# Performance work log

Measured on AMD Instinct MI355X. Metric: run time of the kernel, lower is better.

## Reference

```python
import jax, jax.numpy as jnp
import numpy as np

N = 16000        # nodes
E = 256000       # edges
D_IN = 1280      # input node features
HID = 256        # hidden dim (all hidden_dims equal; required by res_linear shapes)
HEADS = 8
C = HID // HEADS # 32 channels per head
G = 32           # graphs in the batch
O = 64           # output labels (GO terms)
NB = 2           # conv blocks = len(hidden_dims) - 1
EPS = 1e-5


def _bn(h, g, b):
    # eval-mode BatchNorm1d with running_mean=0, running_var=1 (init state)
    return h * (g / jnp.sqrt(1.0 + EPS)) + b


def _seg_softmax(logits, seg, num):
    # numerically-stable segment softmax (PyG softmax semantics)
    m = jax.ops.segment_max(logits, seg, num_segments=num)
    e = jnp.exp(logits - m[seg])
    s = jax.ops.segment_sum(e, seg, num_segments=num)
    return e / (s[seg] + 1e-16)


def setup_inputs() -> dict:
    key = jax.random.key(0)
    ks = jax.random.split(key, 16)
    w = lambda i, sh: jax.random.normal(ks[i], sh, jnp.float32) * 0.05
    return {
        "x": jax.random.normal(ks[0], (N, D_IN), jnp.float32),
        "edge_index": jax.random.randint(ks[1], (2, E), 0, N),
        "batch": jnp.sort(jax.random.randint(ks[2], (N,), 0, G)),
        # feature_proj: Linear -> ReLU -> BN
        "fp_W": w(3, (D_IN, HID)), "fp_b": jnp.zeros(HID),
        "fp_g": jnp.ones(HID), "fp_be": jnp.zeros(HID),
        # GATv2Conv per block: lin_l, lin_r, att, out-bias
        "gat_Wl": w(4, (NB, HID, HID)), "gat_bl": jnp.zeros((NB, HID)),
        "gat_Wr": w(5, (NB, HID, HID)), "gat_br": jnp.zeros((NB, HID)),
        "gat_att": w(6, (NB, HEADS, C)), "gat_bias": jnp.zeros((NB, HID)),
        # GINConv MLP: Linear -> ReLU -> BN
        "gin_W": w(7, (NB, HID, HID)), "gin_b": jnp.zeros((NB, HID)),
        "gin_g": jnp.ones((NB, HID)), "gin_be": jnp.zeros((NB, HID)),
        # PyG LayerNorm (graph mode) affine
        "ln_g": jnp.ones((NB, HID)), "ln_b": jnp.zeros((NB, HID)),
        # residual linears
        "res_W": w(8, (NB, HID, HID)), "res_b": jnp.zeros((NB, HID)),
        # GlobalAttention gate MLP
        "pool_W1": w(9, (HID, HID)), "pool_b1": jnp.zeros(HID),
        "pool_W2": w(10, (HID, 1)), "pool_b2": jnp.zeros(1),
        # O label heads (hierarchy=None -> just the MLP), stacked
        "head_W1": w(11, (O, HID, 256)), "head_b1": jnp.zeros((O, 256)),
        "head_g": jnp.ones((O, 256)), "head_be": jnp.zeros((O, 256)),
        "head_W2": w(12, (O, 256)), "head_b2": jnp.zeros(O),
    }


def reference(x, edge_index, batch, fp_W, fp_b, fp_g, fp_be,
              gat_Wl, gat_bl, gat_Wr, gat_br, gat_att, gat_bias,
              gin_W, gin_b, gin_g, gin_be, ln_g, ln_b, res_W, res_b,
              pool_W1, pool_b1, pool_W2, pool_b2,
              head_W1, head_b1, head_g, head_be, head_W2, head_b2):
    n = x.shape[0]
    # feature_proj (eval: dropout = identity)
    h = _bn(jax.nn.relu(x @ fp_W + fp_b), fp_g, fp_be)

    src0, dst0 = edge_index[0], edge_index[1]
    loop = jnp.arange(n)
    src = jnp.concatenate([src0, loop])  # GATv2 adds self-loops by default
    dst = jnp.concatenate([dst0, loop])

    for i in range(NB):
        # ---- GATv2Conv (no activation after, per original control flow) ----
        xl = (h @ gat_Wl[i] + gat_bl[i]).reshape(n, HEADS, C)
        xr = (h @ gat_Wr[i] + gat_br[i]).reshape(n, HEADS, C)
        msg = xl[src]                                   # [E', H, C]
        eact = jax.nn.leaky_relu(msg + xr[dst], 0.2)
        logit = jnp.einsum('ehc,hc->eh', eact, gat_att[i])
        alpha = _seg_softmax(logit, dst, n)             # [E', H]
        h = jax.ops.segment_sum(alpha[:, :, None] * msg, dst,
                                num_segments=n).reshape(n, HID) + gat_bias[i]
        # ---- GINConv: nn((1+0)*x + sum_neighbors), then leaky_relu ----
        agg = jax.ops.segment_sum(h[src0], dst0, num_segments=n)
        gin = _bn(jax.nn.relu((h + agg) @ gin_W[i] + gin_b[i]), gin_g[i], gin_be[i])
        h = jax.nn.leaky_relu(gin, 0.2)
        # ---- PyG LayerNorm (graph mode, batch=None: global mean/std) + residual ----
        mu = h.mean()
        sd = jnp.std(h)
        ln = (h - mu) / (sd + EPS) * ln_g[i] + ln_b[i]
        h = jax.nn.leaky_relu(ln + (h @ res_W[i] + res_b[i]), 0.2)

    # ---- GlobalAttention pooling ----
    gate = jnp.tanh(h @ pool_W1 + pool_b1) @ pool_W2 + pool_b2   # [N, 1]
    a = _seg_softmax(gate[:, 0], batch, G)
    emb = jax.ops.segment_sum(a[:, None] * h, batch, num_segments=G)  # [G, HID]

    # ---- O label heads (hierarchy None -> MLP only), vectorized ----
    z = jnp.einsum('bd,odh->boh', emb, head_W1) + head_b1[None]
    z = _bn(jax.nn.silu(z), head_g[None], head_be[None])
    out = jnp.einsum('boh,oh->bo', z, head_W2) + head_b2[None]
    return out[:, :, None]  # torch.stack(outputs, dim=1) -> [G, O, 1]
```

## Files before the change

kernel.cpp:

```cpp
#include <hip/hip_runtime.h>
#include <math.h>

#define N_NODES 16000
#define N_EDGES 256000
#define EPE (N_EDGES + N_NODES)
#define DIN 1280
#define HID 256
#define HEADS 8
#define CPH 32
#define NG 32
#define NO 64
#define EPSC 1e-5f
#define SPAD 40

typedef __bf16 bf16;
typedef __attribute__((ext_vector_type(8))) __bf16 bf16x8;
typedef __attribute__((ext_vector_type(4))) float floatx4;

__device__ __forceinline__ float lrelu(float v) { return v > 0.f ? v : 0.2f * v; }
__device__ __forceinline__ float bflo(unsigned int u) { return __uint_as_float(u << 16); }
__device__ __forceinline__ float bfhi(unsigned int u) { return __uint_as_float(u & 0xffff0000u); }
__device__ __forceinline__ unsigned int bfpack(float x, float y) {
    bf16 b0 = (bf16)x, b1 = (bf16)y;
    return ((unsigned int)*(unsigned short*)&b0) | (((unsigned int)*(unsigned short*)&b1) << 16);
}

__device__ __forceinline__ void barrier_lds() {
    asm volatile("s_waitcnt lgkmcnt(0)" ::: "memory");
    __builtin_amdgcn_s_barrier();
}

__global__ void wconv_gen(const float* __restrict__ W, bf16* __restrict__ Wt, int K, int total) {
    int idx = blockIdx.x * 256 + threadIdx.x;
    if (idx >= total) return;
    int per = K * HID;
    int l = idx / per, rem = idx - l * per;
    int n = rem / K, k = rem - n * K;
    Wt[idx] = (bf16)W[(size_t)l * per + (size_t)k * HID + n];
}

__global__ void wconv_pair(const float* __restrict__ Wl, const float* __restrict__ Wr,
                           bf16* __restrict__ Wt) {
    int idx = blockIdx.x * 256 + threadIdx.x;
    int n = idx >> 8, k = idx & 255;
    float v = (n < 256) ? Wl[(size_t)k * HID + n] : Wr[(size_t)k * HID + (n - 256)];
    Wt[idx] = (bf16)v;
}

__global__ __launch_bounds__(256) void gemm128(
    const bf16* __restrict__ A, const bf16* __restrict__ Bt,
    const float* __restrict__ bias, const float* __restrict__ bias2,
    bf16* __restrict__ C, int K, int ldc, int mode,
    const float* __restrict__ g, const float* __restrict__ be,
    float2* __restrict__ statp, const float* __restrict__ stat)
{
    __shared__ __align__(16) bf16 As[2][128 * SPAD];
    __shared__ __align__(16) bf16 Bs[2][128 * SPAD];
    const int tid = threadIdx.x;
    const int bm = blockIdx.y * 128, bn = blockIdx.x * 128;
    const int w = tid >> 6, lane = tid & 63;
    const int wm = (w & 1) * 64, wn = (w >> 1) * 64;
    const int lrow = lane & 15, lk8 = (lane >> 4) * 8;

    floatx4 acc[4][4];
#pragma unroll
    for (int i = 0; i < 4; i++)
#pragma unroll
        for (int j = 0; j < 4; j++) acc[i][j] = (floatx4){0.f, 0.f, 0.f, 0.f};

    const int r2 = tid >> 1, c2 = tid & 1;
    const bf16* gA = A + (size_t)(bm + r2) * K + c2 * 16;
    const bf16* gB = Bt + (size_t)(bn + r2) * K + c2 * 16;
    bf16* sA = &As[0][r2 * SPAD + c2 * 16];
    bf16* sB = &Bs[0][r2 * SPAD + c2 * 16];

    const int nk = K >> 5;
    bf16x8 a[4][2], b[4][2];
#pragma unroll
    for (int u = 0; u < 4; u++) {
        const bf16* pa = gA + u * 32;
        a[u][0] = *(const bf16x8*)(pa + 0);
        a[u][1] = *(const bf16x8*)(pa + 8);
        const bf16* pb = gB + u * 32;
        b[u][0] = *(const bf16x8*)(pb + 0);
        b[u][1] = *(const bf16x8*)(pb + 8);
    }

    for (int it0 = 0; it0 < nk; it0 += 4) {
#pragma unroll
        for (int u = 0; u < 4; u++) {
            const int it = it0 + u;
            const int p = u & 1;
            const int po = p * 128 * SPAD;
            *(bf16x8*)(sA + po + 0) = a[u][0];
            *(bf16x8*)(sA + po + 8) = a[u][1];
            *(bf16x8*)(sB + po + 0) = b[u][0];
            *(bf16x8*)(sB + po + 8) = b[u][1];
            barrier_lds();
            if (it + 4 < nk) {
                const bf16* pa = gA + (it + 4) * 32;
                a[u][0] = *(const bf16x8*)(pa + 0);
                a[u][1] = *(const bf16x8*)(pa + 8);
                const bf16* pb = gB + (it + 4) * 32;
                b[u][0] = *(const bf16x8*)(pb + 0);
                b[u][1] = *(const bf16x8*)(pb + 8);
            }
            bf16x8 af[4], bfr[4];
#pragma unroll
            for (int i = 0; i < 4; i++) af[i] = *(const bf16x8*)&As[p][(wm + 16 * i + lrow) * SPAD + lk8];
#pragma unroll
            for (int j = 0; j < 4; j++) bfr[j] = *(const bf16x8*)&Bs[p][(wn + 16 * j + lrow) * SPAD + lk8];
#pragma unroll
            for (int i = 0; i < 4; i++)
#pragma unroll
                for (int j = 0; j < 4; j++)
                    acc[i][j] = __builtin_amdgcn_mfma_f32_16x16x32_bf16(af[i], bfr[j], acc[i][j], 0, 0, 0);
            barrier_lds();
        }
    }

    const float inv = rsqrtf(1.f + EPSC);
    float mu = 0.f, rs = 0.f;
    if (mode == 3) {
        const float inv_n = 1.f / (float)((size_t)N_NODES * HID);
        mu = stat[0] * inv_n;
        float var = stat[1] * inv_n - mu * mu;
        rs = 1.f / (sqrtf(fmaxf(var, 0.f)) + EPSC);
    }
    float sz = 0.f, sq = 0.f;
#pragma unroll
    for (int j = 0; j < 4; j++) {
        int col = bn + wn + 16 * j + lrow;
        float bcol = (col < HID) ? bias[col] : bias2[col - HID];
        float gc = (mode >= 2) ? g[col] : 0.f;
        float bec = (mode >= 2) ? be[col] : 0.f;
#pragma unroll
        for (int i = 0; i < 4; i++) {
            int row0 = bm + wm + 16 * i + (lane >> 4) * 4;
#pragma unroll
            for (int r = 0; r < 4; r++) {
                float z = acc[i][j][r] + bcol;
                if (mode == 2) {
                    z = fmaxf(z, 0.f) * (gc * inv) + bec;
                    z = lrelu(z);
                    sz += z; sq += z * z;
                } else if (mode == 3) {
                    float h = (float)A[(size_t)(row0 + r) * K + col];
                    z = (h - mu) * rs * gc + bec + z;
                    z = lrelu(z);
                }
                C[(size_t)(row0 + r) * ldc + col] = (bf16)z;
            }
        }
    }
    if (mode == 2) {
        for (int o = 32; o > 0; o >>= 1) { sz += __shfl_down(sz, o); sq += __shfl_down(sq, o); }
        __syncthreads();
        float* rs_ = (float*)&As[0][0];
        float* rq_ = (float*)&Bs[0][0];
        if (lane == 0) { rs_[w] = sz; rq_[w] = sq; }
        __syncthreads();
        if (tid == 0)
            statp[blockIdx.y * gridDim.x + blockIdx.x] =
                make_float2(rs_[0] + rs_[1] + rs_[2] + rs_[3],
                            rq_[0] + rq_[1] + rq_[2] + rq_[3]);
    }
}

__global__ __launch_bounds__(256, 1) void gemm_f32A(
    const float* __restrict__ A, const bf16* __restrict__ Bt,
    const float* __restrict__ bias, bf16* __restrict__ C, int K,
    const float* __restrict__ g, const float* __restrict__ be)
{
    __shared__ __align__(16) bf16 As[2][128 * SPAD];
    __shared__ __align__(16) bf16 Bs[2][128 * SPAD];
    const int tid = threadIdx.x;
    const int bm = blockIdx.y * 128, bn = blockIdx.x * 128;
    const int w = tid >> 6, lane = tid & 63;
    const int wm = (w & 1) * 64, wn = (w >> 1) * 64;
    const int lrow = lane & 15, lk8 = (lane >> 4) * 8;

    floatx4 acc[4][4];
#pragma unroll
    for (int i = 0; i < 4; i++)
#pragma unroll
        for (int j = 0; j < 4; j++) acc[i][j] = (floatx4){0.f, 0.f, 0.f, 0.f};

    const int r2 = tid >> 1, c2 = tid & 1;
    const float* gA = A + (size_t)(bm + r2) * K + c2 * 16;
    const bf16* gB = Bt + (size_t)(bn + r2) * K + c2 * 16;
    bf16* sA = &As[0][r2 * SPAD + c2 * 16];
    bf16* sB = &Bs[0][r2 * SPAD + c2 * 16];

    const int nk = K >> 5;
    float4 a[4][4];
    bf16x8 b[4][2];
#pragma unroll
    for (int u = 0; u < 4; u++) {
        const float* pa = gA + u * 32;
        a[u][0] = *(const float4*)(pa + 0);
        a[u][1] = *(const float4*)(pa + 4);
        a[u][2] = *(const float4*)(pa + 8);
        a[u][3] = *(const float4*)(pa + 12);
        const bf16* pb = gB + u * 32;
        b[u][0] = *(const bf16x8*)(pb + 0);
        b[u][1] = *(const bf16x8*)(pb + 8);
    }

    for (int it0 = 0; it0 < nk; it0 += 4) {
#pragma unroll
        for (int u = 0; u < 4; u++) {
            const int it = it0 + u;
            const int p = u & 1;
            const int po = p * 128 * SPAD;
            bf16x8 h0, h1;
            h0[0] = (bf16)a[u][0].x; h0[1] = (bf16)a[u][0].y; h0[2] = (bf16)a[u][0].z; h0[3] = (bf16)a[u][0].w;
            h0[4] = (bf16)a[u][1].x; h0[5] = (bf16)a[u][1].y; h0[6] = (bf16)a[u][1].z; h0[7] = (bf16)a[u][1].w;
            h1[0] = (bf16)a[u][2].x; h1[1] = (bf16)a[u][2].y; h1[2] = (bf16)a[u][2].z; h1[3] = (bf16)a[u][2].w;
            h1[4] = (bf16)a[u][3].x; h1[5] = (bf16)a[u][3].y; h1[6] = (bf16)a[u][3].z; h1[7] = (bf16)a[u][3].w;
            *(bf16x8*)(sA + po + 0) = h0;
            *(bf16x8*)(sA + po + 8) = h1;
            *(bf16x8*)(sB + po + 0) = b[u][0];
            *(bf16x8*)(sB + po + 8) = b[u][1];
            barrier_lds();
            if (it + 4 < nk) {
                const float* pa = gA + (it + 4) * 32;
                a[u][0] = *(const float4*)(pa + 0);
                a[u][1] = *(const float4*)(pa + 4);
                a[u][2] = *(const float4*)(pa + 8);
                a[u][3] = *(const float4*)(pa + 12);
                const bf16* pb = gB + (it + 4) * 32;
                b[u][0] = *(const bf16x8*)(pb + 0);
                b[u][1] = *(const bf16x8*)(pb + 8);
            }
            bf16x8 af[4], bfr[4];
#pragma unroll
            for (int i = 0; i < 4; i++) af[i] = *(const bf16x8*)&As[p][(wm + 16 * i + lrow) * SPAD + lk8];
#pragma unroll
            for (int j = 0; j < 4; j++) bfr[j] = *(const bf16x8*)&Bs[p][(wn + 16 * j + lrow) * SPAD + lk8];
#pragma unroll
            for (int i = 0; i < 4; i++)
#pragma unroll
                for (int j = 0; j < 4; j++)
                    acc[i][j] = __builtin_amdgcn_mfma_f32_16x16x32_bf16(af[i], bfr[j], acc[i][j], 0, 0, 0);
            barrier_lds();
        }
    }

    const float inv = rsqrtf(1.f + EPSC);
#pragma unroll
    for (int j = 0; j < 4; j++) {
        int col = bn + wn + 16 * j + lrow;
        float bcol = bias[col];
        float gc = g[col] * inv;
        float bec = be[col];
#pragma unroll
        for (int i = 0; i < 4; i++) {
            int row0 = bm + wm + 16 * i + (lane >> 4) * 4;
#pragma unroll
            for (int r = 0; r < 4; r++) {
                float z = fmaxf(acc[i][j][r] + bcol, 0.f) * gc + bec;
                C[(size_t)(row0 + r) * HID + col] = (bf16)z;
            }
        }
    }
}

__global__ void hist_kernel(const int* __restrict__ ei, int* __restrict__ cnt) {
    int e = blockIdx.x * 256 + threadIdx.x;
    if (e >= EPE) return;
    int d = (e < N_EDGES) ? ei[N_EDGES + e] : (e - N_EDGES);
    atomicAdd(&cnt[d], 1);
}

__global__ __launch_bounds__(1024) void scan_kernel(const int* __restrict__ cnt,
                                                    int* __restrict__ roff, int* __restrict__ cursor,
                                                    const int* __restrict__ batch,
                                                    int* __restrict__ gstart) {
    __shared__ int wsum[16];
    int t = threadIdx.x;
    int base = t * 16;
    int local[16]; int s = 0;
#pragma unroll
    for (int i = 0; i < 16; i++) {
        int idx = base + i;
        int v = (idx < N_NODES) ? cnt[idx] : 0;
        local[i] = s; s += v;
    }
    int lane = t & 63, wid = t >> 6;
    int incl = s;
    for (int o = 1; o < 64; o <<= 1) { int v = __shfl_up(incl, o); if (lane >= o) incl += v; }
    if (lane == 63) wsum[wid] = incl;
    __syncthreads();
    if (t == 0) { int a = 0; for (int k = 0; k < 16; k++) { int v = wsum[k]; wsum[k] = a; a += v; } }
    __syncthreads();
    int texcl = incl - s + wsum[wid];
#pragma unroll
    for (int i = 0; i < 16; i++) {
        int idx = base + i;
        if (idx < N_NODES) { int o = texcl + local[i]; roff[idx] = o; cursor[idx] = o; }
    }
    if (t == 1023) roff[N_NODES] = texcl + s;
    if (t <= NG) {
        int lo = 0, hi = N_NODES;
        while (lo < hi) { int mid = (lo + hi) >> 1; if (batch[mid] < t) lo = mid + 1; else hi = mid; }
        gstart[t] = lo;
    }
}

__global__ void scatter_kernel(const int* __restrict__ ei, int* __restrict__ cursor,
                               int* __restrict__ esrc) {
    int e = blockIdx.x * 256 + threadIdx.x;
    if (e >= EPE) return;
    int s, d;
    if (e < N_EDGES) { s = ei[e]; d = ei[N_EDGES + e]; }
    else { s = d = e - N_EDGES; }
    int pos = atomicAdd(&cursor[d], 1);
    esrc[pos] = s;
}

__global__ __launch_bounds__(256) void gat_wave(
    const bf16* __restrict__ XLR, const int* __restrict__ roff, const int* __restrict__ esrc,
    const float* __restrict__ att, const float* __restrict__ gbias, bf16* __restrict__ out)
{
    const int wid = threadIdx.x >> 6;
    const int lane = threadIdx.x & 63;
    const int d = blockIdx.x * 4 + wid;
    const int beg = roff[d], end = roff[d + 1];
    const int c0 = lane * 4;

    const unsigned int* xru = (const unsigned int*)(XLR + (size_t)d * 512 + 256 + c0);
    const unsigned int xr01 = xru[0], xr23 = xru[1];
    const float xr0 = bflo(xr01), xr1 = bfhi(xr01), xr2 = bflo(xr23), xr3 = bfhi(xr23);
    const float at0 = att[c0], at1 = att[c0 + 1], at2 = att[c0 + 2], at3 = att[c0 + 3];

    float m = -INFINITY, s = 0.f;
    float a0 = 0.f, a1 = 0.f, a2 = 0.f, a3 = 0.f;

    int e = beg;
    for (; e + 3 < end; e += 4) {
        int s0 = esrc[e], s1 = esrc[e + 1], s2 = esrc[e + 2], s3 = esrc[e + 3];
        const unsigned int* q0 = (const unsigned int*)(XLR + (size_t)s0 * 512 + c0);
        const unsigned int* q1 = (const unsigned int*)(XLR + (size_t)s1 * 512 + c0);
        const unsigned int* q2 = (const unsigned int*)(XLR + (size_t)s2 * 512 + c0);
        const unsigned int* q3 = (const unsigned int*)(XLR + (size_t)s3 * 512 + c0);
        unsigned int u01 = q0[0], u23 = q0[1];
        unsigned int v01 = q1[0], v23 = q1[1];
        unsigned int w01 = q2[0], w23 = q2[1];
        unsigned int x01 = q3[0], x23 = q3[1];
        float x0 = bflo(u01), x1 = bfhi(u01), x2 = bflo(u23), x3 = bfhi(u23);
        float y0 = bflo(v01), y1 = bfhi(v01), y2 = bflo(v23), y3 = bfhi(v23);
        float z0 = bflo(w01), z1 = bfhi(w01), z2 = bflo(w23), z3 = bfhi(w23);
        float t0 = bflo(x01), t1 = bfhi(x01), t2 = bflo(x23), t3 = bfhi(x23);
        float p0 = lrelu(x0 + xr0) * at0 + lrelu(x1 + xr1) * at1
                 + lrelu(x2 + xr2) * at2 + lrelu(x3 + xr3) * at3;
        float p1 = lrelu(y0 + xr0) * at0 + lrelu(y1 + xr1) * at1
                 + lrelu(y2 + xr2) * at2 + lrelu(y3 + xr3) * at3;
        float p2 = lrelu(z0 + xr0) * at0 + lrelu(z1 + xr1) * at1
                 + lrelu(z2 + xr2) * at2 + lrelu(z3 + xr3) * at3;
        float p3 = lrelu(t0 + xr0) * at0 + lrelu(t1 + xr1) * at1
                 + lrelu(t2 + xr2) * at2 + lrelu(t3 + xr3) * at3;
        p0 += __shfl_xor(p0, 1);  p1 += __shfl_xor(p1, 1);
        p2 += __shfl_xor(p2, 1);  p3 += __shfl_xor(p3, 1);
        p0 += __shfl_xor(p0, 2);  p1 += __shfl_xor(p1, 2);
        p2 += __shfl_xor(p2, 2);  p3 += __shfl_xor(p3, 2);
        p0 += __shfl_xor(p0, 4);  p1 += __shfl_xor(p1, 4);
        p2 += __shfl_xor(p2, 4);  p3 += __shfl_xor(p3, 4);
        float mn = fmaxf(fmaxf(m, fmaxf(p0, p1)), fmaxf(p2, p3));
        float rsc = __expf(m - mn);
        float w0 = __expf(p0 - mn);
        float w1 = __expf(p1 - mn);
        float w2 = __expf(p2 - mn);
        float w3 = __expf(p3 - mn);
        s = s * rsc + (w0 + w1) + (w2 + w3);
        a0 = a0 * rsc + (w0 * x0 + w1 * y0) + (w2 * z0 + w3 * t0);
        a1 = a1 * rsc + (w0 * x1 + w1 * y1) + (w2 * z1 + w3 * t1);
        a2 = a2 * rsc + (w0 * x2 + w1 * y2) + (w2 * z2 + w3 * t2);
        a3 = a3 * rsc + (w0 * x3 + w1 * y3) + (w2 * z3 + w3 * t3);
        m = mn;
    }
    for (; e < end; ++e) {
        int s0 = esrc[e];
        const unsigned int* q0 = (const unsigned int*)(XLR + (size_t)s0 * 512 + c0);
        unsigned int u01 = q0[0], u23 = q0[1];
        float x0 = bflo(u01), x1 = bfhi(u01), x2 = bflo(u23), x3 = bfhi(u23);
        float p = lrelu(x0 + xr0) * at0 + lrelu(x1 + xr1) * at1
                + lrelu(x2 + xr2) * at2 + lrelu(x3 + xr3) * at3;
        p += __shfl_xor(p, 1);
        p += __shfl_xor(p, 2);
        p += __shfl_xor(p, 4);
        float mn = fmaxf(m, p);
        float rsc = __expf(m - mn);
        float wgt = __expf(p - mn);
        s = s * rsc + wgt;
        a0 = a0 * rsc + wgt * x0;
        a1 = a1 * rsc + wgt * x1;
        a2 = a2 * rsc + wgt * x2;
        a3 = a3 * rsc + wgt * x3;
        m = mn;
    }

    const float rinv = 1.f / (s + 1e-16f);
    float v0 = gbias[c0]     + a0 * rinv;
    float v1 = gbias[c0 + 1] + a1 * rinv;
    float v2 = gbias[c0 + 2] + a2 * rinv;
    float v3 = gbias[c0 + 3] + a3 * rinv;
    unsigned int* op = (unsigned int*)(out + (size_t)d * HID + c0);
    op[0] = bfpack(v0, v1);
    op[1] = bfpack(v2, v3);
}

__global__ __launch_bounds__(256) void gin_wave(
    const bf16* __restrict__ H, const int* __restrict__ roff,
    const int* __restrict__ esrc, bf16* __restrict__ U)
{
    const int wid = threadIdx.x >> 6;
    const int lane = threadIdx.x & 63;
    const int d = blockIdx.x * 4 + wid;
    const int beg = roff[d], end = roff[d + 1];
    const int c0 = lane * 4;

    float a0 = 0.f, a1 = 0.f, a2 = 0.f, a3 = 0.f;
    int e = beg;
    for (; e + 3 < end; e += 4) {
        int s0 = esrc[e], s1 = esrc[e + 1], s2 = esrc[e + 2], s3 = esrc[e + 3];
        const unsigned int* p0 = (const unsigned int*)(H + (size_t)s0 * HID + c0);
        const unsigned int* p1 = (const unsigned int*)(H + (size_t)s1 * HID + c0);
        const unsigned int* p2 = (const unsigned int*)(H + (size_t)s2 * HID + c0);
        const unsigned int* p3 = (const unsigned int*)(H + (size_t)s3 * HID + c0);
        unsigned int u01 = p0[0], u23 = p0[1];
        unsigned int v01 = p1[0], v23 = p1[1];
        unsigned int w01 = p2[0], w23 = p2[1];
        unsigned int x01 = p3[0], x23 = p3[1];
        a0 += (bflo(u01) + bflo(v01)) + (bflo(w01) + bflo(x01));
        a1 += (bfhi(u01) + bfhi(v01)) + (bfhi(w01) + bfhi(x01));
        a2 += (bflo(u23) + bflo(v23)) + (bflo(w23) + bflo(x23));
        a3 += (bfhi(u23) + bfhi(v23)) + (bfhi(w23) + bfhi(x23));
    }
    for (; e < end; ++e) {
        const unsigned int* p0 = (const unsigned int*)(H + (size_t)esrc[e] * HID + c0);
        unsigned int u01 = p0[0], u23 = p0[1];
        a0 += bflo(u01); a1 += bfhi(u01); a2 += bflo(u23); a3 += bfhi(u23);
    }
    unsigned int* up = (unsigned int*)(U + (size_t)d * HID + c0);
    up[0] = bfpack(a0, a1);
    up[1] = bfpack(a2, a3);
}

__global__ void stats_reduce(const float2* __restrict__ part, float* __restrict__ stat, int n) {
    int t = threadIdx.x;
    float s = 0.f, q = 0.f;
    for (int i = t; i < n; i += 256) { float2 v = part[i]; s += v.x; q += v.y; }
    for (int o = 32; o > 0; o >>= 1) { s += __shfl_down(s, o); q += __shfl_down(q, o); }
    __shared__ float ls[4], lq[4];
    int wid = t >> 6, lane = t & 63;
    if (lane == 0) { ls[wid] = s; lq[wid] = q; }
    __syncthreads();
    if (t == 0) { stat[0] = ls[0] + ls[1] + ls[2] + ls[3]; stat[1] = lq[0] + lq[1] + lq[2] + lq[3]; }
}

__global__ __launch_bounds__(256) void pool_gate_kernel(const bf16* __restrict__ t,
    const float* __restrict__ W2, const float* __restrict__ b2, float* __restrict__ gate)
{
    int n = blockIdx.x * 4 + (threadIdx.x >> 6);
    int lane = threadIdx.x & 63;
    const bf16* p = t + (size_t)n * HID + lane * 4;
    float4 w = *(const float4*)(W2 + lane * 4);
    float s = tanhf((float)p[0]) * w.x + tanhf((float)p[1]) * w.y
            + tanhf((float)p[2]) * w.z + tanhf((float)p[3]) * w.w;
    for (int o = 32; o > 0; o >>= 1) s += __shfl_down(s, o);
    if (lane == 0) gate[n] = s + b2[0];
}

__global__ __launch_bounds__(256) void pool_stats_kernel(
    float* __restrict__ gate, const int* __restrict__ gstart)
{
    int g = blockIdx.x, t = threadIdx.x;
    int lo = gstart[g], hi = gstart[g + 1];
    __shared__ float red[256];
    float m = -INFINITY;
    for (int n = lo + t; n < hi; n += 256) m = fmaxf(m, gate[n]);
    red[t] = m; __syncthreads();
    for (int st = 128; st > 0; st >>= 1) { if (t < st) red[t] = fmaxf(red[t], red[t + st]); __syncthreads(); }
    m = red[0]; __syncthreads();
    float s = 0.f;
    for (int n = lo + t; n < hi; n += 256) s += __expf(gate[n] - m);
    red[t] = s; __syncthreads();
    for (int st = 128; st > 0; st >>= 1) { if (t < st) red[t] += red[t + st]; __syncthreads(); }
    float sinv = 1.f / (red[0] + 1e-16f);
    for (int n = lo + t; n < hi; n += 256) gate[n] = __expf(gate[n] - m) * sinv;
}

__global__ __launch_bounds__(256) void emb_accum_kernel(
    const float* __restrict__ a, const int* __restrict__ batch,
    const bf16* __restrict__ h, float* __restrict__ emb)
{
    int n0 = blockIdx.x * 32, t = threadIdx.x;
    int cur = batch[n0]; float acc = 0.f;
    for (int j = 0; j < 32; j++) {
        int n = n0 + j;
        int b = batch[n];
        if (b != cur) { atomicAdd(&emb[cur * HID + t], acc); cur = b; acc = 0.f; }
        acc += a[n] * (float)h[(size_t)n * HID + t];
    }
    atomicAdd(&emb[cur * HID + t], acc);
}

__global__ __launch_bounds__(256) void heads_kernel(
    const float* __restrict__ emb, const float* __restrict__ W1, const float* __restrict__ b1,
    const float* __restrict__ hg, const float* __restrict__ hbe, const float* __restrict__ W2,
    const float* __restrict__ b2, float* __restrict__ out)
{
    int o = blockIdx.x;
    int g0 = blockIdx.y * 4;
    int k = threadIdx.x;
    __shared__ float se[4][HID];
    __shared__ float red[256];
#pragma unroll
    for (int j = 0; j < 4; j++) se[j][k] = emb[(g0 + j) * HID + k];
    __syncthreads();
    const float* w1p = W1 + (size_t)o * HID * HID + k;
    float zb = b1[o * HID + k];
    float z0 = zb, z1 = zb, z2 = zb, z3 = zb;
#pragma unroll 8
    for (int d = 0; d < HID; d++) {
        float w = w1p[(size_t)d * HID];
        z0 = fmaf(se[0][d], w, z0);
        z1 = fmaf(se[1][d], w, z1);
        z2 = fmaf(se[2][d], w, z2);
        z3 = fmaf(se[3][d], w, z3);
    }
    const float gk = hg[o * HID + k] * rsqrtf(1.f + EPSC);
    const float bek = hbe[o * HID + k];
    const float w2 = W2[o * HID + k];
    const float b2o = b2[o];
    float zz[4] = {z0, z1, z2, z3};
#pragma unroll
    for (int j = 0; j < 4; j++) {
        float z = zz[j];
        float sil = z / (1.f + expf(-z));
        red[k] = (sil * gk + bek) * w2;
        __syncthreads();
        for (int st = 128; st > 0; st >>= 1) { if (k < st) red[k] += red[k + st]; __syncthreads(); }
        if (k == 0) out[(g0 + j) * NO + o] = red[0] + b2o;
        __syncthreads();
    }
}

extern "C" void kernel_launch(void* const* d_in, const int* in_sizes, int n_in,
                              void* d_out, int out_size, void* d_ws, size_t ws_size,
                              hipStream_t stream) {
    const float* x        = (const float*)d_in[0];
    const int*   ei       = (const int*)  d_in[1];
    const int*   batch    = (const int*)  d_in[2];
    const float* fp_W     = (const float*)d_in[3];
    const float* fp_b     = (const float*)d_in[4];
    const float* fp_g     = (const float*)d_in[5];
    const float* fp_be    = (const float*)d_in[6];
    const float* gat_Wl   = (const float*)d_in[7];
    const float* gat_bl   = (const float*)d_in[8];
    const float* gat_Wr   = (const float*)d_in[9];
    const float* gat_br   = (const float*)d_in[10];
    const float* gat_att  = (const float*)d_in[11];
    const float* gat_bias = (const float*)d_in[12];
    const float* gin_W    = (const float*)d_in[13];
    const float* gin_b    = (const float*)d_in[14];
    const float* gin_g    = (const float*)d_in[15];
    const float* gin_be   = (const float*)d_in[16];
    const float* ln_g     = (const float*)d_in[17];
    const float* ln_b     = (const float*)d_in[18];
    const float* res_W    = (const float*)d_in[19];
    const float* res_b    = (const float*)d_in[20];
    const float* pool_W1  = (const float*)d_in[21];
    const float* pool_b1  = (const float*)d_in[22];
    const float* pool_W2  = (const float*)d_in[23];
    const float* pool_b2  = (const float*)d_in[24];
    const float* head_W1  = (const float*)d_in[25];
    const float* head_b1  = (const float*)d_in[26];
    const float* head_g   = (const float*)d_in[27];
    const float* head_be  = (const float*)d_in[28];
    const float* head_W2  = (const float*)d_in[29];
    const float* head_b2  = (const float*)d_in[30];
    float* out = (float*)d_out;

    char* base = (char*)d_ws;
    size_t off = 0;
    auto alloc = [&](size_t bytes) -> char* {
        char* p = base + off; off += (bytes + 255) & ~(size_t)255; return p;
    };
    int*   esrc   = (int*)  alloc((size_t)EPE * 4);
    int*   cnt    = (int*)  alloc((size_t)N_NODES * 4);
    int*   roff   = (int*)  alloc((size_t)(N_NODES + 1) * 4);
    int*   cursor = (int*)  alloc((size_t)N_NODES * 4);
    float* gate   = (float*)alloc((size_t)N_NODES * 4);
    int*   gstart = (int*)  alloc((NG + 1) * 4);
    float* emb    = (float*)alloc(NG * HID * 4);
    float* stat   = (float*)alloc(8);
    float2* statp = (float2*)alloc(1024 * 8);
    bf16*  Hb0    = (bf16*) alloc((size_t)N_NODES * HID * 2);
    bf16*  Hb1    = (bf16*) alloc((size_t)N_NODES * HID * 2);
    bf16*  XLR    = (bf16*) alloc((size_t)N_NODES * 512 * 2);
    bf16*  fpWt   = (bf16*) alloc((size_t)DIN * HID * 2);
    bf16*  wlrT0  = (bf16*) alloc((size_t)512 * HID * 2);
    bf16*  wlrT1  = (bf16*) alloc((size_t)512 * HID * 2);
    bf16*  gwT    = (bf16*) alloc((size_t)2 * HID * HID * 2);
    bf16*  rwT    = (bf16*) alloc((size_t)2 * HID * HID * 2);
    bf16*  pwT    = (bf16*) alloc((size_t)HID * HID * 2);
    bf16*  Ub     = XLR;
    bf16*  wlrT[2] = { wlrT0, wlrT1 };

    wconv_gen<<<(DIN * HID + 255) / 256, 256, 0, stream>>>(fp_W, fpWt, DIN, DIN * HID);
    wconv_pair<<<512, 256, 0, stream>>>(gat_Wl, gat_Wr, wlrT0);
    wconv_pair<<<512, 256, 0, stream>>>(gat_Wl + HID * HID, gat_Wr + HID * HID, wlrT1);
    wconv_gen<<<512, 256, 0, stream>>>(gin_W, gwT, HID, 2 * HID * HID);
    wconv_gen<<<512, 256, 0, stream>>>(res_W, rwT, HID, 2 * HID * HID);
    wconv_gen<<<256, 256, 0, stream>>>(pool_W1, pwT, HID, HID * HID);

    hipMemsetAsync(cnt, 0, N_NODES * sizeof(int), stream);
    hist_kernel<<<(EPE + 255) / 256, 256, 0, stream>>>(ei, cnt);
    scan_kernel<<<1, 1024, 0, stream>>>(cnt, roff, cursor, batch, gstart);
    scatter_kernel<<<(EPE + 255) / 256, 256, 0, stream>>>(ei, cursor, esrc);

    dim3 gridF(2, 125);
    dim3 g128_256(2, 125);
    dim3 g128_512(4, 125);
    gemm_f32A<<<gridF, 256, 0, stream>>>(x, fpWt, fp_b, Hb0, DIN, fp_g, fp_be);

    bf16* hcur = Hb0;
    bf16* hoth = Hb1;
    for (int i = 0; i < 2; i++) {
        gemm128<<<g128_512, 256, 0, stream>>>(hcur, wlrT[i], gat_bl + i * HID, gat_br + i * HID,
                                              XLR, HID, 512, 0, nullptr, nullptr, nullptr, nullptr);
        gat_wave<<<N_NODES / 4, 256, 0, stream>>>(XLR, roff, esrc, gat_att + i * HEADS * CPH,
                                                  gat_bias + i * HID, hoth);
        gin_wave<<<N_NODES / 4, 256, 0, stream>>>(hoth, roff, esrc, Ub);
        gemm128<<<g128_256, 256, 0, stream>>>(Ub, gwT + (size_t)i * HID * HID, gin_b + i * HID,
                                              nullptr, hcur, HID, HID, 2,
                                              gin_g + i * HID, gin_be + i * HID, statp, nullptr);
        stats_reduce<<<1, 256, 0, stream>>>(statp, stat, 250);
        gemm128<<<g128_256, 256, 0, stream>>>(hcur, rwT + (size_t)i * HID * HID, res_b + i * HID,
                                              nullptr, hoth, HID, HID, 3,
                                              ln_g + i * HID, ln_b + i * HID, nullptr, stat);
        bf16* tmp = hcur; hcur = hoth; hoth = tmp;
    }

    gemm128<<<g128_256, 256, 0, stream>>>(hcur, pwT, pool_b1, nullptr, hoth, HID, HID, 0,
                                          nullptr, nullptr, nullptr, nullptr);
    pool_gate_kernel<<<N_NODES / 4, 256, 0, stream>>>(hoth, pool_W2, pool_b2, gate);
    pool_stats_kernel<<<NG, 256, 0, stream>>>(gate, gstart);
    hipMemsetAsync(emb, 0, NG * HID * sizeof(float), stream);
    emb_accum_kernel<<<N_NODES / 32, 256, 0, stream>>>(gate, batch, hcur, emb);

    dim3 hgrid(NO, 8);
    heads_kernel<<<hgrid, 256, 0, stream>>>(emb, head_W1, head_b1, head_g, head_be,
                                            head_W2, head_b2, out);
}
```

Baseline: 531.3 us.

## Split-K the input projection GEMM and fold stats reduction into atomics

The feature-projection GEMM (K=1280) now runs as a 2-way split-K grid, doubling its block count from 250 to 500. Each half writes fp32 partials, and a separate combine kernel sums them and applies bias, ReLU and BN before packing to bf16. Separately, the LayerNorm statistics reduction kernel is removed: each GEMM block atomically adds its sum and sum of squares into a global stat, which gin_wave zeroes beforehand. The trade-off is extra fp32 partial traffic (about 32MB written and read) and one more launch, against better CU occupancy. Float atomics also make the stats reduction order nondeterministic.

```diff
diff --git a/kernel.cpp b/kernel.cpp
--- a/kernel.cpp
+++ b/kernel.cpp
@@ -12,6 +12,8 @@
 #define NO 64
 #define EPSC 1e-5f
 #define SPAD 40
+#define KSPLIT 2
+#define KHALF (DIN / KSPLIT)
 
 typedef __bf16 bf16;
 typedef __attribute__((ext_vector_type(8))) __bf16 bf16x8;
@@ -52,7 +54,7 @@
     const float* __restrict__ bias, const float* __restrict__ bias2,
     bf16* __restrict__ C, int K, int ldc, int mode,
     const float* __restrict__ g, const float* __restrict__ be,
-    float2* __restrict__ statp, const float* __restrict__ stat)
+    float* __restrict__ stat)
 {
     __shared__ __align__(16) bf16 As[2][128 * SPAD];
     __shared__ __align__(16) bf16 Bs[2][128 * SPAD];
@@ -160,22 +162,22 @@
         float* rq_ = (float*)&Bs[0][0];
         if (lane == 0) { rs_[w] = sz; rq_[w] = sq; }
         __syncthreads();
-        if (tid == 0)
-            statp[blockIdx.y * gridDim.x + blockIdx.x] =
-                make_float2(rs_[0] + rs_[1] + rs_[2] + rs_[3],
-                            rq_[0] + rq_[1] + rq_[2] + rq_[3]);
-    }
-}
-
-__global__ __launch_bounds__(256, 1) void gemm_f32A(
+        if (tid == 0) {
+            atomicAdd(&stat[0], rs_[0] + rs_[1] + rs_[2] + rs_[3]);
+            atomicAdd(&stat[1], rq_[0] + rq_[1] + rq_[2] + rq_[3]);
+        }
+    }
+}
+
+__global__ __launch_bounds__(256) void gemm_f32A_split(
     const float* __restrict__ A, const bf16* __restrict__ Bt,
-    const float* __restrict__ bias, bf16* __restrict__ C, int K,
-    const float* __restrict__ g, const float* __restrict__ be)
+    float* __restrict__ P, int K)
 {
     __shared__ __align__(16) bf16 As[2][128 * SPAD];
     __shared__ __align__(16) bf16 Bs[2][128 * SPAD];
     const int tid = threadIdx.x;
     const int bm = blockIdx.y * 128, bn = blockIdx.x * 128;
+    const int kz = blockIdx.z;
     const int w = tid >> 6, lane = tid & 63;
     const int wm = (w & 1) * 64, wn = (w >> 1) * 64;
     const int lrow = lane & 15, lk8 = (lane >> 4) * 8;
@@ -187,12 +189,12 @@
         for (int j = 0; j < 4; j++) acc[i][j] = (floatx4){0.f, 0.f, 0.f, 0.f};
 
     const int r2 = tid >> 1, c2 = tid & 1;
-    const float* gA = A + (size_t)(bm + r2) * K + c2 * 16;
-    const bf16* gB = Bt + (size_t)(bn + r2) * K + c2 * 16;
+    const float* gA = A + (size_t)(bm + r2) * K + kz * KHALF + c2 * 16;
+    const bf16* gB = Bt + (size_t)(bn + r2) * K + kz * KHALF + c2 * 16;
     bf16* sA = &As[0][r2 * SPAD + c2 * 16];
     bf16* sB = &Bs[0][r2 * SPAD + c2 * 16];
 
-    const int nk = K >> 5;
+    const int nk = KHALF >> 5;
     float4 a[4][4];
     bf16x8 b[4][2];
 #pragma unroll
@@ -247,23 +249,41 @@
         }
     }
 
-    const float inv = rsqrtf(1.f + EPSC);
+    float* Pz = P + (size_t)kz * N_NODES * HID;
 #pragma unroll
     for (int j = 0; j < 4; j++) {
         int col = bn + wn + 16 * j + lrow;
-        float bcol = bias[col];
-        float gc = g[col] * inv;
-        float bec = be[col];
 #pragma unroll
         for (int i = 0; i < 4; i++) {
             int row0 = bm + wm + 16 * i + (lane >> 4) * 4;
 #pragma unroll
-            for (int r = 0; r < 4; r++) {
-                float z = fmaxf(acc[i][j][r] + bcol, 0.f) * gc + bec;
-                C[(size_t)(row0 + r) * HID + col] = (bf16)z;
-            }
+            for (int r = 0; r < 4; r++)
+                Pz[(size_t)(row0 + r) * HID + col] = acc[i][j][r];
         }
     }
+}
+
+__global__ __launch_bounds__(256) void fp_combine(
+    const float* __restrict__ P, const float* __restrict__ bias,
+    const float* __restrict__ g, const float* __restrict__ be, bf16* __restrict__ C)
+{
+    const float inv = rsqrtf(1.f + EPSC);
+    int idx = blockIdx.x * 256 + threadIdx.x;
+    const int total = N_NODES * HID / 4;
+    if (idx >= total) return;
+    float4 p0 = ((const float4*)P)[idx];
+    float4 p1 = ((const float4*)(P + (size_t)N_NODES * HID))[idx];
+    int col4 = (idx & 63) * 4;
+    float4 bv = *(const float4*)(bias + col4);
+    float4 gv = *(const float4*)(g + col4);
+    float4 ev = *(const float4*)(be + col4);
+    float z0 = fmaxf(p0.x + p1.x + bv.x, 0.f) * (gv.x * inv) + ev.x;
+    float z1 = fmaxf(p0.y + p1.y + bv.y, 0.f) * (gv.y * inv) + ev.y;
+    float z2 = fmaxf(p0.z + p1.z + bv.z, 0.f) * (gv.z * inv) + ev.z;
+    float z3 = fmaxf(p0.w + p1.w + bv.w, 0.f) * (gv.w * inv) + ev.w;
+    unsigned int* op = (unsigned int*)(C + (size_t)idx * 4);
+    op[0] = bfpack(z0, z1);
+    op[1] = bfpack(z2, z3);
 }
 
 __global__ void hist_kernel(const int* __restrict__ ei, int* __restrict__ cnt) {
@@ -412,8 +432,9 @@
 
 __global__ __launch_bounds__(256) void gin_wave(
     const bf16* __restrict__ H, const int* __restrict__ roff,
-    const int* __restrict__ esrc, bf16* __restrict__ U)
-{
+    const int* __restrict__ esrc, bf16* __restrict__ U, float* __restrict__ stat)
+{
+    if (blockIdx.x == 0 && threadIdx.x == 0) { stat[0] = 0.f; stat[1] = 0.f; }
     const int wid = threadIdx.x >> 6;
     const int lane = threadIdx.x & 63;
     const int d = blockIdx.x * 4 + wid;
@@ -445,18 +466,6 @@
     unsigned int* up = (unsigned int*)(U + (size_t)d * HID + c0);
     up[0] = bfpack(a0, a1);
     up[1] = bfpack(a2, a3);
-}
-
-__global__ void stats_reduce(const float2* __restrict__ part, float* __restrict__ stat, int n) {
-    int t = threadIdx.x;
-    float s = 0.f, q = 0.f;
-    for (int i = t; i < n; i += 256) { float2 v = part[i]; s += v.x; q += v.y; }
-    for (int o = 32; o > 0; o >>= 1) { s += __shfl_down(s, o); q += __shfl_down(q, o); }
-    __shared__ float ls[4], lq[4];
-    int wid = t >> 6, lane = t & 63;
-    if (lane == 0) { ls[wid] = s; lq[wid] = q; }
-    __syncthreads();
-    if (t == 0) { stat[0] = ls[0] + ls[1] + ls[2] + ls[3]; stat[1] = lq[0] + lq[1] + lq[2] + lq[3]; }
 }
 
 __global__ __launch_bounds__(256) void pool_gate_kernel(const bf16* __restrict__ t,
@@ -596,7 +605,7 @@
     int*   gstart = (int*)  alloc((NG + 1) * 4);
     float* emb    = (float*)alloc(NG * HID * 4);
     float* stat   = (float*)alloc(8);
-    float2* statp = (float2*)alloc(1024 * 8);
+    float* Pbuf   = (float*)alloc((size_t)KSPLIT * N_NODES * HID * 4);
     bf16*  Hb0    = (bf16*) alloc((size_t)N_NODES * HID * 2);
     bf16*  Hb1    = (bf16*) alloc((size_t)N_NODES * HID * 2);
     bf16*  XLR    = (bf16*) alloc((size_t)N_NODES * 512 * 2);
@@ -621,31 +630,31 @@
     scan_kernel<<<1, 1024, 0, stream>>>(cnt, roff, cursor, batch, gstart);
     scatter_kernel<<<(EPE + 255) / 256, 256, 0, stream>>>(ei, cursor, esrc);
 
-    dim3 gridF(2, 125);
+    dim3 gridF(2, 125, KSPLIT);
     dim3 g128_256(2, 125);
     dim3 g128_512(4, 125);
-    gemm_f32A<<<gridF, 256, 0, stream>>>(x, fpWt, fp_b, Hb0, DIN, fp_g, fp_be);
+    gemm_f32A_split<<<gridF, 256, 0, stream>>>(x, fpWt, Pbuf, DIN);
+    fp_combine<<<(N_NODES * HID / 4 + 255) / 256, 256, 0, stream>>>(Pbuf, fp_b, fp_g, fp_be, Hb0);
 
     bf16* hcur = Hb0;
     bf16* hoth = Hb1;
     for (int i = 0; i < 2; i++) {
         gemm128<<<g128_512, 256, 0, stream>>>(hcur, wlrT[i], gat_bl + i * HID, gat_br + i * HID,
-                                              XLR, HID, 512, 0, nullptr, nullptr, nullptr, nullptr);
+                                              XLR, HID, 512, 0, nullptr, nullptr, nullptr);
         gat_wave<<<N_NODES / 4, 256, 0, stream>>>(XLR, roff, esrc, gat_att + i * HEADS * CPH,
                                                   gat_bias + i * HID, hoth);
-        gin_wave<<<N_NODES / 4, 256, 0, stream>>>(hoth, roff, esrc, Ub);
+        gin_wave<<<N_NODES / 4, 256, 0, stream>>>(hoth, roff, esrc, Ub, stat);
         gemm128<<<g128_256, 256, 0, stream>>>(Ub, gwT + (size_t)i * HID * HID, gin_b + i * HID,
                                               nullptr, hcur, HID, HID, 2,
-                                              gin_g + i * HID, gin_be + i * HID, statp, nullptr);
-        stats_reduce<<<1, 256, 0, stream>>>(statp, stat, 250);
+                                              gin_g + i * HID, gin_be + i * HID, stat);
         gemm128<<<g128_256, 256, 0, stream>>>(hcur, rwT + (size_t)i * HID * HID, res_b + i * HID,
                                               nullptr, hoth, HID, HID, 3,
-                                              ln_g + i * HID, ln_b + i * HID, nullptr, stat);
+                                              ln_g + i * HID, ln_b + i * HID, stat);
         bf16* tmp = hcur; hcur = hoth; hoth = tmp;
     }
 
     gemm128<<<g128_256, 256, 0, stream>>>(hcur, pwT, pool_b1, nullptr, hoth, HID, HID, 0,
-                                          nullptr, nullptr, nullptr, nullptr);
+                                          nullptr, nullptr, nullptr);
     pool_gate_kernel<<<N_NODES / 4, 256, 0, stream>>>(hoth, pool_W2, pool_b2, gate);
     pool_stats_kernel<<<NG, 256, 0, stream>>>(gate, gstart);
     hipMemsetAsync(emb, 0, NG * HID * sizeof(float), stream);
```

Result: slower. 544.0 us (+2.4%).

## Fold LayerNorm stats reduction into GEMM atomics and restructure label heads kernel

Applied to the files above, without the earlier changes.

Removes the separate stats_reduce launch. The mode-2 GIN GEMM now adds its per-block sum and sum-of-squares straight into a global stat buffer with atomics, and gin_wave zeroes that buffer first. The heads kernel now uses one block per label covering all 32 graphs, so each head_W1 column is read once instead of eight times. Its block-wide tree reductions become wave shuffles. The trade-offs are non-deterministic float atomic ordering, more registers (32 accumulators per thread) and fewer blocks (64) in the heads kernel.

```diff
diff --git a/kernel.cpp b/kernel.cpp
--- a/kernel.cpp
+++ b/kernel.cpp
@@ -52,7 +52,7 @@
     const float* __restrict__ bias, const float* __restrict__ bias2,
     bf16* __restrict__ C, int K, int ldc, int mode,
     const float* __restrict__ g, const float* __restrict__ be,
-    float2* __restrict__ statp, const float* __restrict__ stat)
+    float* __restrict__ stat)
 {
     __shared__ __align__(16) bf16 As[2][128 * SPAD];
     __shared__ __align__(16) bf16 Bs[2][128 * SPAD];
@@ -160,10 +160,10 @@
         float* rq_ = (float*)&Bs[0][0];
         if (lane == 0) { rs_[w] = sz; rq_[w] = sq; }
         __syncthreads();
-        if (tid == 0)
-            statp[blockIdx.y * gridDim.x + blockIdx.x] =
-                make_float2(rs_[0] + rs_[1] + rs_[2] + rs_[3],
-                            rq_[0] + rq_[1] + rq_[2] + rq_[3]);
+        if (tid == 0) {
+            atomicAdd(&stat[0], rs_[0] + rs_[1] + rs_[2] + rs_[3]);
+            atomicAdd(&stat[1], rq_[0] + rq_[1] + rq_[2] + rq_[3]);
+        }
     }
 }
 
@@ -412,8 +412,9 @@
 
 __global__ __launch_bounds__(256) void gin_wave(
     const bf16* __restrict__ H, const int* __restrict__ roff,
-    const int* __restrict__ esrc, bf16* __restrict__ U)
-{
+    const int* __restrict__ esrc, bf16* __restrict__ U, float* __restrict__ stat)
+{
+    if (blockIdx.x == 0 && threadIdx.x == 0) { stat[0] = 0.f; stat[1] = 0.f; }
     const int wid = threadIdx.x >> 6;
     const int lane = threadIdx.x & 63;
     const int d = blockIdx.x * 4 + wid;
@@ -447,18 +448,6 @@
     up[1] = bfpack(a2, a3);
 }
 
-__global__ void stats_reduce(const float2* __restrict__ part, float* __restrict__ stat, int n) {
-    int t = threadIdx.x;
-    float s = 0.f, q = 0.f;
-    for (int i = t; i < n; i += 256) { float2 v = part[i]; s += v.x; q += v.y; }
-    for (int o = 32; o > 0; o >>= 1) { s += __shfl_down(s, o); q += __shfl_down(q, o); }
-    __shared__ float ls[4], lq[4];
-    int wid = t >> 6, lane = t & 63;
-    if (lane == 0) { ls[wid] = s; lq[wid] = q; }
-    __syncthreads();
-    if (t == 0) { stat[0] = ls[0] + ls[1] + ls[2] + ls[3]; stat[1] = lq[0] + lq[1] + lq[2] + lq[3]; }
-}
-
 __global__ __launch_bounds__(256) void pool_gate_kernel(const bf16* __restrict__ t,
     const float* __restrict__ W2, const float* __restrict__ b2, float* __restrict__ gate)
 {
@@ -511,40 +500,51 @@
     const float* __restrict__ hg, const float* __restrict__ hbe, const float* __restrict__ W2,
     const float* __restrict__ b2, float* __restrict__ out)
 {
-    int o = blockIdx.x;
-    int g0 = blockIdx.y * 4;
-    int k = threadIdx.x;
-    __shared__ float se[4][HID];
-    __shared__ float red[256];
-#pragma unroll
-    for (int j = 0; j < 4; j++) se[j][k] = emb[(g0 + j) * HID + k];
+    const int o = blockIdx.x;
+    const int k = threadIdx.x;
+    __shared__ float se[NG][HID];
+    __shared__ float part[NG][4];
+#pragma unroll
+    for (int i = 0; i < 8; i++)
+        ((float4*)&se[0][0])[k + i * 256] = ((const float4*)emb)[k + i * 256];
     __syncthreads();
+
     const float* w1p = W1 + (size_t)o * HID * HID + k;
-    float zb = b1[o * HID + k];
-    float z0 = zb, z1 = zb, z2 = zb, z3 = zb;
-#pragma unroll 8
-    for (int d = 0; d < HID; d++) {
-        float w = w1p[(size_t)d * HID];
-        z0 = fmaf(se[0][d], w, z0);
-        z1 = fmaf(se[1][d], w, z1);
-        z2 = fmaf(se[2][d], w, z2);
-        z3 = fmaf(se[3][d], w, z3);
-    }
+    const float zb = b1[o * HID + k];
+    float acc[NG];
+#pragma unroll
+    for (int j = 0; j < NG; j++) acc[j] = zb;
+
+    for (int d4 = 0; d4 < HID / 4; d4++) {
+        float w0 = w1p[(size_t)(d4 * 4 + 0) * HID];
+        float w1v = w1p[(size_t)(d4 * 4 + 1) * HID];
+        float w2v = w1p[(size_t)(d4 * 4 + 2) * HID];
+        float w3v = w1p[(size_t)(d4 * 4 + 3) * HID];
+#pragma unroll
+        for (int j = 0; j < NG; j++) {
+            float4 s4 = *(const float4*)&se[j][d4 * 4];
+            acc[j] = fmaf(s4.x, w0, acc[j]);
+            acc[j] = fmaf(s4.y, w1v, acc[j]);
+            acc[j] = fmaf(s4.z, w2v, acc[j]);
+            acc[j] = fmaf(s4.w, w3v, acc[j]);
+        }
+    }
+
     const float gk = hg[o * HID + k] * rsqrtf(1.f + EPSC);
     const float bek = hbe[o * HID + k];
     const float w2 = W2[o * HID + k];
-    const float b2o = b2[o];
-    float zz[4] = {z0, z1, z2, z3};
-#pragma unroll
-    for (int j = 0; j < 4; j++) {
-        float z = zz[j];
+    const int wid = k >> 6, lane = k & 63;
+#pragma unroll
+    for (int j = 0; j < NG; j++) {
+        float z = acc[j];
         float sil = z / (1.f + expf(-z));
-        red[k] = (sil * gk + bek) * w2;
-        __syncthreads();
-        for (int st = 128; st > 0; st >>= 1) { if (k < st) red[k] += red[k + st]; __syncthreads(); }
-        if (k == 0) out[(g0 + j) * NO + o] = red[0] + b2o;
-        __syncthreads();
-    }
+        float v = (sil * gk + bek) * w2;
+        for (int off = 32; off > 0; off >>= 1) v += __shfl_down(v, off);
+        if (lane == 0) part[j][wid] = v;
+    }
+    __syncthreads();
+    if (k < NG)
+        out[k * NO + o] = part[k][0] + part[k][1] + part[k][2] + part[k][3] + b2[o];
 }
 
 extern "C" void kernel_launch(void* const* d_in, const int* in_sizes, int n_in,
@@ -596,7 +596,6 @@
     int*   gstart = (int*)  alloc((NG + 1) * 4);
     float* emb    = (float*)alloc(NG * HID * 4);
     float* stat   = (float*)alloc(8);
-    float2* statp = (float2*)alloc(1024 * 8);
     bf16*  Hb0    = (bf16*) alloc((size_t)N_NODES * HID * 2);
     bf16*  Hb1    = (bf16*) alloc((size_t)N_NODES * HID * 2);
     bf16*  XLR    = (bf16*) alloc((size_t)N_NODES * 512 * 2);
@@ -630,28 +629,26 @@
     bf16* hoth = Hb1;
     for (int i = 0; i < 2; i++) {
         gemm128<<<g128_512, 256, 0, stream>>>(hcur, wlrT[i], gat_bl + i * HID, gat_br + i * HID,
-                                              XLR, HID, 512, 0, nullptr, nullptr, nullptr, nullptr);
+                                              XLR, HID, 512, 0, nullptr, nullptr, nullptr);
         gat_wave<<<N_NODES / 4, 256, 0, stream>>>(XLR, roff, esrc, gat_att + i * HEADS * CPH,
                                                   gat_bias + i * HID, hoth);
-        gin_wave<<<N_NODES / 4, 256, 0, stream>>>(hoth, roff, esrc, Ub);
+        gin_wave<<<N_NODES / 4, 256, 0, stream>>>(hoth, roff, esrc, Ub, stat);
         gemm128<<<g128_256, 256, 0, stream>>>(Ub, gwT + (size_t)i * HID * HID, gin_b + i * HID,
                                               nullptr, hcur, HID, HID, 2,
-                                              gin_g + i * HID, gin_be + i * HID, statp, nullptr);
-        stats_reduce<<<1, 256, 0, stream>>>(statp, stat, 250);
+                                              gin_g + i * HID, gin_be + i * HID, stat);
         gemm128<<<g128_256, 256, 0, stream>>>(hcur, rwT + (size_t)i * HID * HID, res_b + i * HID,
                                               nullptr, hoth, HID, HID, 3,
-                                              ln_g + i * HID, ln_b + i * HID, nullptr, stat);
+                                              ln_g + i * HID, ln_b + i * HID, stat);
         bf16* tmp = hcur; hcur = hoth; hoth = tmp;
     }
 
     gemm128<<<g128_256, 256, 0, stream>>>(hcur, pwT, pool_b1, nullptr, hoth, HID, HID, 0,
-                                          nullptr, nullptr, nullptr, nullptr);
+                                          nullptr, nullptr, nullptr);
     pool_gate_kernel<<<N_NODES / 4, 256, 0, stream>>>(hoth, pool_W2, pool_b2, gate);
     pool_stats_kernel<<<NG, 256, 0, stream>>>(gate, gstart);
     hipMemsetAsync(emb, 0, NG * HID * sizeof(float), stream);
     emb_accum_kernel<<<N_NODES / 32, 256, 0, stream>>>(gate, batch, hcur, emb);
 
-    dim3 hgrid(NO, 8);
-    heads_kernel<<<hgrid, 256, 0, stream>>>(emb, head_W1, head_b1, head_g, head_be,
-                                            head_W2, head_b2, out);
-}
+    heads_kernel<<<NO, 256, 0, stream>>>(emb, head_W1, head_b1, head_g, head_be,
+                                         head_W2, head_b2, out);
+}
```

New measurement: 596.3 us. 12.2% more time.
